# Performance work log

Hardware: AMD Instinct MI355X
Metric: run time of the kernel (lower is better)

## Reference

```python
import jax, jax.numpy as jnp
import numpy as np

B, C, N = 8, 128, 256          # batch, descriptor dim, num points
DIMS = [2 * C, 512, 256, 64, 1]  # [input_dim] + cfg.layers + [1]
EPS = 1e-5


def setup_inputs() -> dict:
    key = jax.random.key(0)
    ks = jax.random.split(key, 32)
    inp = {"x": jax.random.normal(ks[0], (B, C, N), dtype=jnp.float32)}
    ki = 1
    for li in range(4):
        cin, cout = DIMS[li], DIMS[li + 1]
        inp[f"W{li+1}"] = jax.random.normal(ks[ki], (cout, cin), dtype=jnp.float32) / np.sqrt(cin); ki += 1
        inp[f"b{li+1}"] = jnp.zeros((cout,), dtype=jnp.float32)
        if li < 3:  # BatchNorm only on hidden layers
            inp[f"g{li+1}"] = jnp.ones((cout,), dtype=jnp.float32)
            inp[f"be{li+1}"] = jnp.zeros((cout,), dtype=jnp.float32)
            inp[f"m{li+1}"] = 0.1 * jax.random.normal(ks[ki], (cout,), dtype=jnp.float32); ki += 1
            inp[f"v{li+1}"] = 0.5 + jax.random.uniform(ks[ki], (cout,), dtype=jnp.float32); ki += 1
    return inp


def _bn(h, g, be, m, v):
    # inference-mode BatchNorm1d over channel axis of (b, c, p)
    scale = (g * jax.lax.rsqrt(v + EPS))[None, :, None]
    return (h - m[None, :, None]) * scale + be[None, :, None]


def _conv1x1(h, W, b):
    # Conv1d kernel_size=1 == channel matmul: (o,c),(b,c,p)->(b,o,p)
    return jnp.einsum('oc,bcp->bop', W, h) + b[None, :, None]


def reference(x, W1, b1, g1, be1, m1, v1, W2, b2, g2, be2, m2, v2,
              W3, b3, g3, be3, m3, v3, W4, b4):
    b, c, n = x.shape
    # pairwise concat: inputs[:, :, i*n+j] = cat(x[:,:,i], x[:,:,j])
    xi = jnp.broadcast_to(x[:, :, :, None], (b, c, n, n))  # varies with i
    xj = jnp.broadcast_to(x[:, :, None, :], (b, c, n, n))  # varies with j
    pair = jnp.concatenate([xi, xj], axis=1).reshape(b, 2 * c, n * n)
    h = jax.nn.relu(_bn(_conv1x1(pair, W1, b1), g1, be1, m1, v1))
    h = jax.nn.relu(_bn(_conv1x1(h, W2, b2), g2, be2, m2, v2))
    h = jax.nn.relu(_bn(_conv1x1(h, W3, b3), g3, be3, m3, v3))
    h = _conv1x1(h, W4, b4)
    return jax.nn.sigmoid(h)  # (b, 1, n*n) == edges_pred
```

## Files before the change

### kernel.cpp

```cpp
#include <hip/hip_runtime.h>
#include <hip/hip_bf16.h>
#include <hip/hip_fp16.h>

typedef _Float16 f16x8 __attribute__((ext_vector_type(8)));
typedef _Float16 f16x4 __attribute__((ext_vector_type(4)));
typedef float    f32x4 __attribute__((ext_vector_type(4)));

#define EPSV 1e-5f

__global__ void prep_consts(
    const float* __restrict__ b1, const float* __restrict__ g1, const float* __restrict__ be1,
    const float* __restrict__ m1, const float* __restrict__ v1,
    const float* __restrict__ b2, const float* __restrict__ g2, const float* __restrict__ be2,
    const float* __restrict__ m2, const float* __restrict__ v2,
    const float* __restrict__ b3, const float* __restrict__ g3, const float* __restrict__ be3,
    const float* __restrict__ m3, const float* __restrict__ v3,
    float* __restrict__ sc1, float* __restrict__ sh1,
    float* __restrict__ sc2, float* __restrict__ sh2,
    float* __restrict__ sc3, float* __restrict__ sh3) {
  int t = threadIdx.x;
  if (t < 512) { float s = g1[t] * rsqrtf(v1[t] + EPSV); sc1[t] = s; sh1[t] = be1[t] + (b1[t] - m1[t]) * s; }
  if (t < 256) { float s = g2[t] * rsqrtf(v2[t] + EPSV); sc2[t] = s; sh2[t] = be2[t] + (b2[t] - m2[t]) * s; }
  if (t < 64)  { float s = g3[t] * rsqrtf(v3[t] + EPSV); sc3[t] = s; sh3[t] = be3[t] + (b3[t] - m3[t]) * s; }
}

__global__ void prep_convert(const float* __restrict__ W2, const float* __restrict__ W3,
                             _Float16* __restrict__ W2T, _Float16* __restrict__ W3h) {
  int tid = blockIdx.x * 256 + threadIdx.x;
  {
    int lane = tid & 63, cg = (tid >> 6) & 15, ks = tid >> 10;
    int ch = cg * 16 + (lane & 15);
    int k  = ks * 32 + (lane >> 4) * 8;
    const float* src = W2 + (size_t)ch * 512 + k;
    f16x8 v;
    #pragma unroll
    for (int e = 0; e < 8; ++e) v[e] = (_Float16)src[e];
    *(f16x8*)(W2T + (size_t)tid * 8) = v;
  }
  W3h[tid] = (_Float16)W3[tid];
}

__global__ void prep_ab(const float* __restrict__ x, const float* __restrict__ W1,
                        const float* __restrict__ sc1, const float* __restrict__ sh1,
                        _Float16* __restrict__ Ap, _Float16* __restrict__ Bp) {
  int b  = blockIdx.x >> 7;
  int og = blockIdx.x & 127;
  int i  = threadIdx.x;
  float accA[4] = {0.f, 0.f, 0.f, 0.f};
  float accB[4] = {0.f, 0.f, 0.f, 0.f};
  const float* xb  = x  + (size_t)b * 128 * 256 + i;
  const float* w1r = W1 + (size_t)og * 4 * 256;
  for (int c = 0; c < 128; ++c) {
    float xa = xb[c * 256];
    #pragma unroll
    for (int oo = 0; oo < 4; ++oo) {
      accA[oo] = fmaf(w1r[oo * 256 + c],       xa, accA[oo]);
      accB[oo] = fmaf(w1r[oo * 256 + 128 + c], xa, accB[oo]);
    }
  }
  f16x4 oa, ob;
  {
    int o0 = og * 4;
    float4 s = *(const float4*)(sc1 + o0);
    float4 h = *(const float4*)(sh1 + o0);
    oa[0] = (_Float16)(accA[0] * s.x + h.x); oa[1] = (_Float16)(accA[1] * s.y + h.y);
    oa[2] = (_Float16)(accA[2] * s.z + h.z); oa[3] = (_Float16)(accA[3] * s.w + h.w);
    ob[0] = (_Float16)(accB[0] * s.x); ob[1] = (_Float16)(accB[1] * s.y);
    ob[2] = (_Float16)(accB[2] * s.z); ob[3] = (_Float16)(accB[3] * s.w);
  }
  size_t base = ((size_t)(b * 256 + i) << 9) + og * 4;
  *(f16x4*)(Ap + base) = oa;
  *(f16x4*)(Bp + base) = ob;
}

struct alignas(16) Smem {
  union {
    struct { _Float16 sA[8][552]; _Float16 sB[16][552]; } s2;
    struct { _Float16 h2[64][264]; float part[4][64]; } e;
  } u;
};

__global__ __launch_bounds__(512, 4) void edge_main(
    const _Float16* __restrict__ Ap, const _Float16* __restrict__ Bp,
    const _Float16* __restrict__ W2T, const _Float16* __restrict__ W3h,
    const float* __restrict__ sc2, const float* __restrict__ sh2,
    const float* __restrict__ sc3, const float* __restrict__ sh3,
    const float* __restrict__ W4, const float* __restrict__ b4,
    float* __restrict__ out) {
  __shared__ Smem sm;
  const int blk = blockIdx.x;
  const int b  = blk >> 9;
  const int it = (blk >> 4) & 31;
  const int jt = blk & 15;
  const int i0 = it * 8, j0 = jt * 16;

  const int t    = threadIdx.x;
  const int w    = t >> 6;
  const int lane = t & 63;
  const int llo  = lane & 15;
  const int lhi  = lane >> 4;
  const int chQ  = w & 3;
  const int ptH  = w >> 2;

  if (t < 256) {
    int r = t >> 5, c = (t & 31) * 16;
    const _Float16* src = Ap + ((size_t)(b * 256 + i0 + r) << 9) + c;
    *(f16x8*)&sm.u.s2.sA[r][c]     = *(const f16x8*)(src);
    *(f16x8*)&sm.u.s2.sA[r][c + 8] = *(const f16x8*)(src + 8);
  } else {
    int tt = t - 256;
    int r = tt >> 4, c = (tt & 15) * 32;
    const _Float16* src = Bp + ((size_t)(b * 256 + j0 + r) << 9) + c;
    #pragma unroll
    for (int s = 0; s < 4; ++s)
      *(f16x8*)&sm.u.s2.sB[r][c + s * 8] = *(const f16x8*)(src + s * 8);
  }

  const f32x4 vzero = {0.f, 0.f, 0.f, 0.f};
  f32x4 acc[4][4];
  #pragma unroll
  for (int mt = 0; mt < 4; ++mt)
    #pragma unroll
    for (int nt = 0; nt < 4; ++nt) acc[mt][nt] = vzero;

  const f16x8 z8 = {};
  const _Float16* w2p = W2T + chQ * 2048 + lane * 8;

  __syncthreads();

  #pragma unroll 2
  for (int ks = 0; ks < 16; ++ks) {
    f16x8 af[4];
    #pragma unroll
    for (int mt = 0; mt < 4; ++mt)
      af[mt] = *(const f16x8*)(w2p + mt * 512);
    w2p += 8192;

    const int k0 = ks * 32 + lhi * 8;
    f16x8 bv = *(const f16x8*)&sm.u.s2.sB[llo][k0];
    f16x8 bfr[4];
    #pragma unroll
    for (int nt = 0; nt < 4; ++nt) {
      f16x8 av = *(const f16x8*)&sm.u.s2.sA[ptH * 4 + nt][k0];
      f16x8 sv = av + bv;
      bfr[nt] = __builtin_elementwise_max(sv, z8);
    }

    __builtin_amdgcn_s_setprio(1);
    #pragma unroll
    for (int mt = 0; mt < 4; ++mt)
      #pragma unroll
      for (int nt = 0; nt < 4; ++nt)
        acc[mt][nt] = __builtin_amdgcn_mfma_f32_16x16x32_f16(af[mt], bfr[nt], acc[mt][nt], 0, 0, 0);
    __builtin_amdgcn_s_setprio(0);
  }

  __syncthreads();

  #pragma unroll
  for (int pass = 0; pass < 2; ++pass) {
    if (ptH == pass) {
      #pragma unroll
      for (int mt = 0; mt < 4; ++mt) {
        int ch = chQ * 64 + mt * 16 + lhi * 4;
        float4 s = *(const float4*)(sc2 + ch);
        float4 h = *(const float4*)(sh2 + ch);
        #pragma unroll
        for (int nt = 0; nt < 4; ++nt) {
          int pt = nt * 16 + llo;
          f32x4 a = acc[mt][nt];
          f16x4 hb;
          hb[0] = (_Float16)fmaxf(fmaf(a[0], s.x, h.x), 0.f);
          hb[1] = (_Float16)fmaxf(fmaf(a[1], s.y, h.y), 0.f);
          hb[2] = (_Float16)fmaxf(fmaf(a[2], s.z, h.z), 0.f);
          hb[3] = (_Float16)fmaxf(fmaf(a[3], s.w, h.w), 0.f);
          *(f16x4*)&sm.u.e.h2[pt][ch] = hb;
        }
      }
    }
    __syncthreads();

    {
      const int chF = w & 3, ptS = w >> 2;
      f32x4 acc3[2];
      acc3[0] = vzero; acc3[1] = vzero;
      const _Float16* w3p = W3h + (size_t)(chF * 16 + llo) * 256 + lhi * 8;
      #pragma unroll
      for (int k8 = 0; k8 < 8; ++k8) {
        f16x8 a3 = *(const f16x8*)(w3p + k8 * 32);
        #pragma unroll
        for (int q2 = 0; q2 < 2; ++q2) {
          f16x8 b3 = *(const f16x8*)&sm.u.e.h2[(ptS * 2 + q2) * 16 + llo][k8 * 32 + lhi * 8];
          acc3[q2] = __builtin_amdgcn_mfma_f32_16x16x32_f16(a3, b3, acc3[q2], 0, 0, 0);
        }
      }
      int ch3 = chF * 16 + lhi * 4;
      float4 s  = *(const float4*)(sc3 + ch3);
      float4 h  = *(const float4*)(sh3 + ch3);
      float4 wv = *(const float4*)(W4 + ch3);
      #pragma unroll
      for (int q2 = 0; q2 < 2; ++q2) {
        float p = fmaxf(fmaf(acc3[q2][0], s.x, h.x), 0.f) * wv.x
                + fmaxf(fmaf(acc3[q2][1], s.y, h.y), 0.f) * wv.y
                + fmaxf(fmaf(acc3[q2][2], s.z, h.z), 0.f) * wv.z
                + fmaxf(fmaf(acc3[q2][3], s.w, h.w), 0.f) * wv.w;
        p += __shfl_xor(p, 16);
        p += __shfl_xor(p, 32);
        if (lane < 16) sm.u.e.part[chF][(ptS * 2 + q2) * 16 + llo] = p;
      }
    }
    __syncthreads();

    if (t < 64) {
      float tot = sm.u.e.part[0][t] + sm.u.e.part[1][t] + sm.u.e.part[2][t]
                + sm.u.e.part[3][t] + b4[0];
      float sg = 1.f / (1.f + __expf(-tot));
      int il = 4 * pass + (t >> 4), jl = t & 15;
      out[(size_t)b * 65536 + (size_t)(i0 + il) * 256 + (j0 + jl)] = sg;
    }
    __syncthreads();
  }
}

extern "C" void kernel_launch(void* const* d_in, const int* in_sizes, int n_in,
                              void* d_out, int out_size, void* d_ws, size_t ws_size,
                              hipStream_t stream) {
  const float* x   = (const float*)d_in[0];
  const float* W1  = (const float*)d_in[1];
  const float* b1  = (const float*)d_in[2];
  const float* g1  = (const float*)d_in[3];
  const float* be1 = (const float*)d_in[4];
  const float* m1  = (const float*)d_in[5];
  const float* v1  = (const float*)d_in[6];
  const float* W2  = (const float*)d_in[7];
  const float* b2  = (const float*)d_in[8];
  const float* g2  = (const float*)d_in[9];
  const float* be2 = (const float*)d_in[10];
  const float* m2  = (const float*)d_in[11];
  const float* v2  = (const float*)d_in[12];
  const float* W3  = (const float*)d_in[13];
  const float* b3  = (const float*)d_in[14];
  const float* g3  = (const float*)d_in[15];
  const float* be3 = (const float*)d_in[16];
  const float* m3  = (const float*)d_in[17];
  const float* v3  = (const float*)d_in[18];
  const float* W4  = (const float*)d_in[19];
  const float* b4  = (const float*)d_in[20];

  _Float16* Ap = (_Float16*)d_ws;
  _Float16* Bp = Ap + 1048576;
  float* sc1 = (float*)(Bp + 1048576);
  float* sh1 = sc1 + 512;
  float* sc2 = sh1 + 512;
  float* sh2 = sc2 + 256;
  float* sc3 = sh2 + 256;
  float* sh3 = sc3 + 64;
  _Float16* W2T = (_Float16*)(sh3 + 64);
  _Float16* W3h = W2T + 131072;

  prep_consts<<<1, 512, 0, stream>>>(b1, g1, be1, m1, v1, b2, g2, be2, m2, v2,
                                     b3, g3, be3, m3, v3, sc1, sh1, sc2, sh2, sc3, sh3);
  prep_convert<<<64, 256, 0, stream>>>(W2, W3, W2T, W3h);
  prep_ab<<<1024, 256, 0, stream>>>(x, W1, sc1, sh1, Ap, Bp);
  edge_main<<<4096, 512, 0, stream>>>(Ap, Bp, W2T, W3h, sc2, sh2, sc3, sh3, W4, b4, (float*)d_out);
}
```

Before: 189.7 us.

## Shrink edge tile to 8x8 pairs with 4 waves and double-buffered W2 fragments

```diff
diff --git a/kernel.cpp b/kernel.cpp
--- a/kernel.cpp
+++ b/kernel.cpp
@@ -75,12 +75,12 @@
 
 struct alignas(16) Smem {
   union {
-    struct { _Float16 sA[8][552]; _Float16 sB[16][552]; } s2;
+    struct { _Float16 sA[8][552]; _Float16 sB[8][552]; } s2;
     struct { _Float16 h2[64][264]; float part[4][64]; } e;
   } u;
 };
 
-__global__ __launch_bounds__(512, 4) void edge_main(
+__global__ __launch_bounds__(256, 3) void edge_main(
     const _Float16* __restrict__ Ap, const _Float16* __restrict__ Bp,
     const _Float16* __restrict__ W2T, const _Float16* __restrict__ W3h,
     const float* __restrict__ sc2, const float* __restrict__ sh2,
@@ -89,26 +89,27 @@
     float* __restrict__ out) {
   __shared__ Smem sm;
   const int blk = blockIdx.x;
-  const int b  = blk >> 9;
-  const int it = (blk >> 4) & 31;
-  const int jt = blk & 15;
-  const int i0 = it * 8, j0 = jt * 16;
+  const int b  = blk >> 10;
+  const int it = (blk >> 5) & 31;
+  const int jt = blk & 31;
+  const int i0 = it * 8, j0 = jt * 8;
 
   const int t    = threadIdx.x;
   const int w    = t >> 6;
   const int lane = t & 63;
   const int llo  = lane & 15;
   const int lhi  = lane >> 4;
-  const int chQ  = w & 3;
-  const int ptH  = w >> 2;
-
-  if (t < 256) {
-    int r = t >> 5, c = (t & 31) * 16;
+  const int gj   = llo & 7;
+  const int giOff= llo >> 3;
+
+  if (t < 128) {
+    int r = t >> 4, c = (t & 15) * 32;
     const _Float16* src = Ap + ((size_t)(b * 256 + i0 + r) << 9) + c;
-    *(f16x8*)&sm.u.s2.sA[r][c]     = *(const f16x8*)(src);
-    *(f16x8*)&sm.u.s2.sA[r][c + 8] = *(const f16x8*)(src + 8);
+    #pragma unroll
+    for (int s = 0; s < 4; ++s)
+      *(f16x8*)&sm.u.s2.sA[r][c + s * 8] = *(const f16x8*)(src + s * 8);
   } else {
-    int tt = t - 256;
+    int tt = t - 128;
     int r = tt >> 4, c = (tt & 15) * 32;
     const _Float16* src = Bp + ((size_t)(b * 256 + j0 + r) << 9) + c;
     #pragma unroll
@@ -124,101 +125,106 @@
     for (int nt = 0; nt < 4; ++nt) acc[mt][nt] = vzero;
 
   const f16x8 z8 = {};
-  const _Float16* w2p = W2T + chQ * 2048 + lane * 8;
-
-  __syncthreads();
-
-  #pragma unroll 2
-  for (int ks = 0; ks < 16; ++ks) {
-    f16x8 af[4];
-    #pragma unroll
-    for (int mt = 0; mt < 4; ++mt)
-      af[mt] = *(const f16x8*)(w2p + mt * 512);
-    w2p += 8192;
-
-    const int k0 = ks * 32 + lhi * 8;
-    f16x8 bv = *(const f16x8*)&sm.u.s2.sB[llo][k0];
-    f16x8 bfr[4];
+  const _Float16* w2base = W2T + w * 2048 + lane * 8;
+
+#define LOAD_AF(dst, kk)                                                     \
+  {                                                                          \
+    const _Float16* _p = w2base + (kk) * 8192;                               \
+    _Pragma("unroll")                                                        \
+    for (int mt = 0; mt < 4; ++mt)                                           \
+      dst[mt] = *(const f16x8*)(_p + mt * 512);                              \
+  }
+
+#define KSTEP(afv, kk)                                                       \
+  {                                                                          \
+    const int k0 = (kk) * 32 + lhi * 8;                                      \
+    f16x8 bv = *(const f16x8*)&sm.u.s2.sB[gj][k0];                           \
+    f16x8 bfr[4];                                                            \
+    _Pragma("unroll")                                                        \
+    for (int nt = 0; nt < 4; ++nt) {                                         \
+      f16x8 av = *(const f16x8*)&sm.u.s2.sA[nt * 2 + giOff][k0];             \
+      f16x8 sv = av + bv;                                                    \
+      bfr[nt] = __builtin_elementwise_max(sv, z8);                           \
+    }                                                                        \
+    _Pragma("unroll")                                                        \
+    for (int mt = 0; mt < 4; ++mt)                                           \
+      _Pragma("unroll")                                                      \
+      for (int nt = 0; nt < 4; ++nt)                                         \
+        acc[mt][nt] = __builtin_amdgcn_mfma_f32_16x16x32_f16(                \
+            afv[mt], bfr[nt], acc[mt][nt], 0, 0, 0);                         \
+  }
+
+  f16x8 afA[4], afB[4];
+  LOAD_AF(afA, 0);
+
+  __syncthreads();
+
+  for (int ks = 0; ks < 16; ks += 2) {
+    LOAD_AF(afB, ks + 1);
+    KSTEP(afA, ks);
+    if (ks + 2 < 16) LOAD_AF(afA, ks + 2);
+    KSTEP(afB, ks + 1);
+  }
+#undef LOAD_AF
+#undef KSTEP
+
+  __syncthreads();
+
+  #pragma unroll
+  for (int mt = 0; mt < 4; ++mt) {
+    int ch = w * 64 + mt * 16 + lhi * 4;
+    float4 s = *(const float4*)(sc2 + ch);
+    float4 h = *(const float4*)(sh2 + ch);
     #pragma unroll
     for (int nt = 0; nt < 4; ++nt) {
-      f16x8 av = *(const f16x8*)&sm.u.s2.sA[ptH * 4 + nt][k0];
-      f16x8 sv = av + bv;
-      bfr[nt] = __builtin_elementwise_max(sv, z8);
-    }
-
-    __builtin_amdgcn_s_setprio(1);
-    #pragma unroll
-    for (int mt = 0; mt < 4; ++mt)
+      int pt = nt * 16 + llo;
+      f32x4 a = acc[mt][nt];
+      f16x4 hb;
+      hb[0] = (_Float16)fmaxf(fmaf(a[0], s.x, h.x), 0.f);
+      hb[1] = (_Float16)fmaxf(fmaf(a[1], s.y, h.y), 0.f);
+      hb[2] = (_Float16)fmaxf(fmaf(a[2], s.z, h.z), 0.f);
+      hb[3] = (_Float16)fmaxf(fmaf(a[3], s.w, h.w), 0.f);
+      *(f16x4*)&sm.u.e.h2[pt][ch] = hb;
+    }
+  }
+  __syncthreads();
+
+  {
+    f32x4 acc3[4];
+    #pragma unroll
+    for (int nt = 0; nt < 4; ++nt) acc3[nt] = vzero;
+    const _Float16* w3p = W3h + (size_t)(w * 16 + llo) * 256 + lhi * 8;
+    #pragma unroll
+    for (int k8 = 0; k8 < 8; ++k8) {
+      f16x8 a3 = *(const f16x8*)(w3p + k8 * 32);
       #pragma unroll
-      for (int nt = 0; nt < 4; ++nt)
-        acc[mt][nt] = __builtin_amdgcn_mfma_f32_16x16x32_f16(af[mt], bfr[nt], acc[mt][nt], 0, 0, 0);
-    __builtin_amdgcn_s_setprio(0);
-  }
-
-  __syncthreads();
-
-  #pragma unroll
-  for (int pass = 0; pass < 2; ++pass) {
-    if (ptH == pass) {
-      #pragma unroll
-      for (int mt = 0; mt < 4; ++mt) {
-        int ch = chQ * 64 + mt * 16 + lhi * 4;
-        float4 s = *(const float4*)(sc2 + ch);
-        float4 h = *(const float4*)(sh2 + ch);
-        #pragma unroll
-        for (int nt = 0; nt < 4; ++nt) {
-          int pt = nt * 16 + llo;
-          f32x4 a = acc[mt][nt];
-          f16x4 hb;
-          hb[0] = (_Float16)fmaxf(fmaf(a[0], s.x, h.x), 0.f);
-          hb[1] = (_Float16)fmaxf(fmaf(a[1], s.y, h.y), 0.f);
-          hb[2] = (_Float16)fmaxf(fmaf(a[2], s.z, h.z), 0.f);
-          hb[3] = (_Float16)fmaxf(fmaf(a[3], s.w, h.w), 0.f);
-          *(f16x4*)&sm.u.e.h2[pt][ch] = hb;
-        }
+      for (int nt = 0; nt < 4; ++nt) {
+        f16x8 b3 = *(const f16x8*)&sm.u.e.h2[nt * 16 + llo][k8 * 32 + lhi * 8];
+        acc3[nt] = __builtin_amdgcn_mfma_f32_16x16x32_f16(a3, b3, acc3[nt], 0, 0, 0);
       }
     }
-    __syncthreads();
-
-    {
-      const int chF = w & 3, ptS = w >> 2;
-      f32x4 acc3[2];
-      acc3[0] = vzero; acc3[1] = vzero;
-      const _Float16* w3p = W3h + (size_t)(chF * 16 + llo) * 256 + lhi * 8;
-      #pragma unroll
-      for (int k8 = 0; k8 < 8; ++k8) {
-        f16x8 a3 = *(const f16x8*)(w3p + k8 * 32);
-        #pragma unroll
-        for (int q2 = 0; q2 < 2; ++q2) {
-          f16x8 b3 = *(const f16x8*)&sm.u.e.h2[(ptS * 2 + q2) * 16 + llo][k8 * 32 + lhi * 8];
-          acc3[q2] = __builtin_amdgcn_mfma_f32_16x16x32_f16(a3, b3, acc3[q2], 0, 0, 0);
-        }
-      }
-      int ch3 = chF * 16 + lhi * 4;
-      float4 s  = *(const float4*)(sc3 + ch3);
-      float4 h  = *(const float4*)(sh3 + ch3);
-      float4 wv = *(const float4*)(W4 + ch3);
-      #pragma unroll
-      for (int q2 = 0; q2 < 2; ++q2) {
-        float p = fmaxf(fmaf(acc3[q2][0], s.x, h.x), 0.f) * wv.x
-                + fmaxf(fmaf(acc3[q2][1], s.y, h.y), 0.f) * wv.y
-                + fmaxf(fmaf(acc3[q2][2], s.z, h.z), 0.f) * wv.z
-                + fmaxf(fmaf(acc3[q2][3], s.w, h.w), 0.f) * wv.w;
-        p += __shfl_xor(p, 16);
-        p += __shfl_xor(p, 32);
-        if (lane < 16) sm.u.e.part[chF][(ptS * 2 + q2) * 16 + llo] = p;
-      }
-    }
-    __syncthreads();
-
-    if (t < 64) {
-      float tot = sm.u.e.part[0][t] + sm.u.e.part[1][t] + sm.u.e.part[2][t]
-                + sm.u.e.part[3][t] + b4[0];
-      float sg = 1.f / (1.f + __expf(-tot));
-      int il = 4 * pass + (t >> 4), jl = t & 15;
-      out[(size_t)b * 65536 + (size_t)(i0 + il) * 256 + (j0 + jl)] = sg;
-    }
-    __syncthreads();
+    int ch3 = w * 16 + lhi * 4;
+    float4 s  = *(const float4*)(sc3 + ch3);
+    float4 h  = *(const float4*)(sh3 + ch3);
+    float4 wv = *(const float4*)(W4 + ch3);
+    #pragma unroll
+    for (int nt = 0; nt < 4; ++nt) {
+      float p = fmaxf(fmaf(acc3[nt][0], s.x, h.x), 0.f) * wv.x
+              + fmaxf(fmaf(acc3[nt][1], s.y, h.y), 0.f) * wv.y
+              + fmaxf(fmaf(acc3[nt][2], s.z, h.z), 0.f) * wv.z
+              + fmaxf(fmaf(acc3[nt][3], s.w, h.w), 0.f) * wv.w;
+      p += __shfl_xor(p, 16);
+      p += __shfl_xor(p, 32);
+      if (lane < 16) sm.u.e.part[w][nt * 16 + llo] = p;
+    }
+  }
+  __syncthreads();
+
+  if (t < 64) {
+    float tot = sm.u.e.part[0][t] + sm.u.e.part[1][t] + sm.u.e.part[2][t]
+              + sm.u.e.part[3][t] + b4[0];
+    float sg = 1.f / (1.f + __expf(-tot));
+    out[(size_t)b * 65536 + (size_t)(i0 + (t >> 3)) * 256 + (j0 + (t & 7))] = sg;
   }
 }
 
@@ -262,5 +268,5 @@
                                      b3, g3, be3, m3, v3, sc1, sh1, sc2, sh2, sc3, sh3);
   prep_convert<<<64, 256, 0, stream>>>(W2, W3, W2T, W3h);
   prep_ab<<<1024, 256, 0, stream>>>(x, W1, sc1, sh1, Ap, Bp);
-  edge_main<<<4096, 512, 0, stream>>>(Ap, Bp, W2T, W3h, sc2, sh2, sc3, sh3, W4, b4, (float*)d_out);
-}
+  edge_main<<<8192, 256, 0, stream>>>(Ap, Bp, W2T, W3h, sc2, sh2, sc3, sh3, W4, b4, (float*)d_out);
+}
```

Measured after the change: 180.5 us. 1.05x faster.
